# Performance work log

Hardware: AMD Instinct MI355X
Metric: run time of the kernel (lower is better)

The kernel has to match this reference:

```python
import jax, jax.numpy as jnp
import numpy as np

HIDDEN = 2048
NUM_HEAD = 32
GROUP = 8
HEAD_DIM = HIDDEN // NUM_HEAD  # 64
REP = NUM_HEAD // GROUP        # 4


def setup_inputs() -> dict:
    key = jax.random.key(0)
    ks = jax.random.split(key, 9)
    s = 0.02
    kv_dim = GROUP * HEAD_DIM
    return {
        "hidden_states": jax.random.normal(ks[0], (2, 2048, HIDDEN), dtype=jnp.float32),
        "Wq": jax.random.normal(ks[1], (HIDDEN, HIDDEN), dtype=jnp.float32) * s,
        "bq": jnp.zeros((HIDDEN,), dtype=jnp.float32),
        "Wk": jax.random.normal(ks[2], (HIDDEN, kv_dim), dtype=jnp.float32) * s,
        "bk": jnp.zeros((kv_dim,), dtype=jnp.float32),
        "Wv": jax.random.normal(ks[3], (HIDDEN, kv_dim), dtype=jnp.float32) * s,
        "bv": jnp.zeros((kv_dim,), dtype=jnp.float32),
        "Wo": jax.random.normal(ks[4], (HIDDEN, HIDDEN), dtype=jnp.float32) * s,
        "bo": jnp.zeros((HIDDEN,), dtype=jnp.float32),
    }


def reference(hidden_states, Wq, bq, Wk, bk, Wv, bv, Wo, bo):
    B, S, H = hidden_states.shape
    q = hidden_states @ Wq + bq                      # [B,S,H]
    k = hidden_states @ Wk + bk                      # [B,S,G*hd]
    v = hidden_states @ Wv + bv
    q = q.reshape(B, S, NUM_HEAD, HEAD_DIM).transpose(0, 2, 1, 3)   # [B,nh,S,hd]
    k = k.reshape(B, S, GROUP, HEAD_DIM).transpose(0, 2, 1, 3)      # [B,G,S,hd]
    v = v.reshape(B, S, GROUP, HEAD_DIM).transpose(0, 2, 1, 3)
    # expand KV heads: each group head repeated REP times contiguously
    k = jnp.repeat(k, REP, axis=1)                   # [B,nh,S,hd]
    v = jnp.repeat(v, REP, axis=1)
    scale = 1.0 / jnp.sqrt(jnp.float32(HEAD_DIM))
    scores = jnp.einsum("bhqd,bhkd->bhqk", q, k) * scale  # [B,nh,S,S]
    attn = jax.nn.softmax(scores, axis=-1)
    out = jnp.einsum("bhqk,bhkd->bhqd", attn, v)     # [B,nh,S,hd]
    out = out.transpose(0, 2, 1, 3).reshape(B, S, NUM_HEAD * HEAD_DIM)
    return out @ Wo + bo
```

## Files before the change

kernel.cpp:

```cpp
#include <hip/hip_runtime.h>
#include <hip/hip_bf16.h>

typedef __attribute__((ext_vector_type(8))) short bf16x8;
typedef __attribute__((ext_vector_type(4))) short bf16x4;
typedef __attribute__((ext_vector_type(4))) float f32x4;

__device__ __forceinline__ unsigned short f2bf(float f) {
  union { float f; unsigned int u; } v; v.f = f;
  unsigned int r = (v.u + 0x7fffu + ((v.u >> 16) & 1u)) >> 16;
  return (unsigned short)r;
}

__device__ __forceinline__ unsigned int pk2bf(float a, float b) {
  float2 t; t.x = a; t.y = b;
  __hip_bfloat162 h = __float22bfloat162_rn(t);
  union { __hip_bfloat162 h; unsigned int u; } cv; cv.h = h;
  return cv.u;
}

__device__ __forceinline__ void g2l16(unsigned short* lds, const unsigned short* g) {
  __builtin_amdgcn_global_load_lds(
      (const __attribute__((address_space(1))) unsigned int*)g,
      (__attribute__((address_space(3))) unsigned int*)lds, 16, 0, 0);
}


__global__ __launch_bounds__(256) void cast_hs_kernel(const float* __restrict__ in,
                                                      unsigned short* __restrict__ out) {
  size_t i = (size_t)blockIdx.x * 256 + threadIdx.x;
  float4 v = ((const float4*)in)[i];
  ushort4 o;
  o.x = f2bf(v.x); o.y = f2bf(v.y); o.z = f2bf(v.z); o.w = f2bf(v.w);
  ((ushort4*)out)[i] = o;
}

__global__ __launch_bounds__(256) void transpose_cast_kernel(const float* __restrict__ src,
                                                             unsigned short* __restrict__ dst,
                                                             int N) {
  __shared__ float tile[32][33];
  int n0 = blockIdx.x * 32, k0 = blockIdx.y * 32;
  int t = threadIdx.x;
  for (int i = 0; i < 4; ++i) {
    int linear = i * 256 + t;
    int kr = linear >> 5, nc = linear & 31;
    tile[kr][nc] = src[(size_t)(k0 + kr) * N + (n0 + nc)];
  }
  __syncthreads();
  for (int i = 0; i < 4; ++i) {
    int linear = i * 256 + t;
    int nr = linear >> 5, kc = linear & 31;
    dst[(size_t)(n0 + nr) * 2048 + (k0 + kc)] = f2bf(tile[kc][nr]);
  }
}


#define QSCALE 0.18033688011112042f

__global__ __launch_bounds__(256) void gemm_qkv_kernel(
    const unsigned short* __restrict__ A, const unsigned short* __restrict__ Bt,
    const float* __restrict__ bq, const float* __restrict__ bk, const float* __restrict__ bv,
    unsigned short* __restrict__ Qb, unsigned short* __restrict__ Kb,
    unsigned short* __restrict__ Vtb) {
  __shared__ __align__(16) unsigned short smem[128 * 136];
  unsigned short* sA = smem;
  unsigned short* sB = smem + 4096;
  const int K = 2048;
  int bm0 = blockIdx.y * 128, bn0 = blockIdx.x * 128;
  int t = threadIdx.x;
  int w = t >> 6, lane = t & 63, l16 = lane & 15, quad = lane >> 4;
  int wm = (w & 1) * 64, wn = (w >> 1) * 64;
  f32x4 zero = {0.f, 0.f, 0.f, 0.f};
  f32x4 acc[4][4];
  for (int mt = 0; mt < 4; ++mt)
    for (int nt = 0; nt < 4; ++nt) acc[mt][nt] = zero;

  for (int k0 = 0; k0 < K; k0 += 32) {
    for (int i = 0; i < 2; ++i) {
      int linear = i * 256 + t;
      int row = linear >> 2, kofs = (linear & 3) * 8;
      g2l16(sA + linear * 8, A + (size_t)(bm0 + row) * K + k0 + kofs);
      g2l16(sB + linear * 8, Bt + (size_t)(bn0 + row) * K + k0 + kofs);
    }
    __syncthreads();
    bf16x8 af[4], bfr[4];
    for (int mt = 0; mt < 4; ++mt)
      af[mt] = *(const bf16x8*)(sA + (wm + mt * 16 + l16) * 32 + quad * 8);
    for (int nt = 0; nt < 4; ++nt)
      bfr[nt] = *(const bf16x8*)(sB + (wn + nt * 16 + l16) * 32 + quad * 8);
    for (int mt = 0; mt < 4; ++mt)
      for (int nt = 0; nt < 4; ++nt)
        acc[mt][nt] = __builtin_amdgcn_mfma_f32_16x16x32_bf16(af[mt], bfr[nt], acc[mt][nt], 0, 0, 0);
    __syncthreads();
  }

  const int SP = 136;
  bool isV = (bn0 >= 2560);
  bool isQ = (bn0 < 2048);
  const float* bias = isQ ? bq : (bn0 < 2560 ? bk : bv);
  int nbase = isQ ? 0 : (bn0 < 2560 ? 2048 : 2560);

  for (int nt = 0; nt < 4; ++nt) {
    int nl = wn + nt * 16 + l16;
    float bb = bias[bn0 + nl - nbase];
    for (int mt = 0; mt < 4; ++mt)
      for (int r = 0; r < 4; ++r) {
        int ml = wm + mt * 16 + quad * 4 + r;
        float fv = acc[mt][nt][r] + bb;
        if (isQ) fv *= QSCALE;
        unsigned short val = f2bf(fv);
        if (isV) smem[nl * SP + ml] = val;
        else     smem[ml * SP + nl] = val;
      }
  }
  __syncthreads();

  int b = bm0 >> 11, s0 = bm0 & 2047;
  if (bn0 < 2048) {
    for (int i = 0; i < 8; ++i) {
      int idx = i * 256 + t;
      int sub = idx >> 10, s_l = (idx >> 3) & 127, dch = (idx & 7) * 8;
      bf16x8 v = *(const bf16x8*)(smem + s_l * SP + sub * 64 + dch);
      int n = bn0 + sub * 64 + dch;
      int h = n >> 6, d = n & 63;
      *(bf16x8*)(Qb + (((size_t)b * 32 + h) * 2048 + s0 + s_l) * 64 + d) = v;
    }
  } else if (bn0 < 2560) {
    for (int i = 0; i < 8; ++i) {
      int idx = i * 256 + t;
      int sub = idx >> 10, s_l = (idx >> 3) & 127, dch = (idx & 7) * 8;
      bf16x8 v = *(const bf16x8*)(smem + s_l * SP + sub * 64 + dch);
      int nn = bn0 + sub * 64 + dch - 2048;
      int g = nn >> 6, d = nn & 63;
      *(bf16x8*)(Kb + (((size_t)b * 8 + g) * 2048 + s0 + s_l) * 64 + d) = v;
    }
  } else {
    for (int i = 0; i < 8; ++i) {
      int idx = i * 256 + t;
      int nl = idx >> 4, sj = (idx & 15) * 8;
      bf16x8 v = *(const bf16x8*)(smem + nl * SP + sj);
      int nn = bn0 + nl - 2560;
      int g = nn >> 6, d = nn & 63;
      *(bf16x8*)(Vtb + (((size_t)b * 8 + g) * 64 + d) * 2048 + s0 + sj) = v;
    }
  }
}


__global__ __launch_bounds__(256) void attn_kernel(
    const unsigned short* __restrict__ Qb, const unsigned short* __restrict__ Kb,
    const unsigned short* __restrict__ Vtb, unsigned short* __restrict__ AttnB) {
  __shared__ __align__(16) unsigned short Kt[64 * 64];
  __shared__ __align__(16) unsigned short Vt[64 * 64];
  int qt = blockIdx.x, h = blockIdx.y, b = blockIdx.z;
  int g = h >> 2;
  int t = threadIdx.x, w = t >> 6, lane = t & 63, l16 = lane & 15, quad = lane >> 4;

  const unsigned short* qbase =
      Qb + (((size_t)b * 32 + h) * 2048 + qt * 64 + w * 16 + l16) * 64 + quad * 8;
  bf16x8 aQ0 = *(const bf16x8*)(qbase);
  bf16x8 aQ1 = *(const bf16x8*)(qbase + 32);

  const unsigned short* kbase = Kb + ((size_t)b * 8 + g) * (2048 * 64);
  const unsigned short* vbase = Vtb + ((size_t)b * 8 + g) * (64 * 2048);

  float l_acc = 0.f;
  f32x4 zero = {0.f, 0.f, 0.f, 0.f};
  f32x4 o[4];
  for (int dt = 0; dt < 4; ++dt) o[dt] = zero;

  for (int kb = 0; kb < 32; ++kb) {
    for (int i = 0; i < 2; ++i) {
      int linear = i * 256 + t;
      int row = linear & 63, c = linear >> 6;
      g2l16(Kt + linear * 8, kbase + (size_t)(kb * 64 + row) * 64 + c * 8);
      g2l16(Vt + linear * 8, vbase + (size_t)row * 2048 + kb * 64 + c * 8);
    }
    __syncthreads();

    for (int nt = 0; nt < 4; ++nt) {
      bf16x8 bk0 = *(const bf16x8*)(Kt + (quad * 64 + nt * 16 + l16) * 8);
      bf16x8 bk1 = *(const bf16x8*)(Kt + ((quad + 4) * 64 + nt * 16 + l16) * 8);
      f32x4 st = __builtin_amdgcn_mfma_f32_16x16x32_bf16(bk0, aQ0, zero, 0, 0, 0);
      st = __builtin_amdgcn_mfma_f32_16x16x32_bf16(bk1, aQ1, st, 0, 0, 0);

      float p0 = __builtin_amdgcn_exp2f(st[0] - 10.0f);
      float p1 = __builtin_amdgcn_exp2f(st[1] - 10.0f);
      float p2 = __builtin_amdgcn_exp2f(st[2] - 10.0f);
      float p3 = __builtin_amdgcn_exp2f(st[3] - 10.0f);
      l_acc += (p0 + p1) + (p2 + p3);

      union { unsigned int u[2]; bf16x4 v; } pa;
      pa.u[0] = pk2bf(p0, p1);
      pa.u[1] = pk2bf(p2, p3);

      int c = nt * 2 + (quad >> 1);
      int ho = (quad & 1) * 4;
      for (int dt = 0; dt < 4; ++dt) {
        bf16x4 bv = *(const bf16x4*)(Vt + (c * 64 + dt * 16 + l16) * 8 + ho);
        o[dt] = __builtin_amdgcn_mfma_f32_16x16x16bf16_1k(pa.v, bv, o[dt], 0, 0, 0);
      }
    }
    __syncthreads();
  }

  l_acc += __shfl_xor(l_acc, 16);
  l_acc += __shfl_xor(l_acc, 32);

  for (int r = 0; r < 4; ++r) {
    float lr = __shfl(l_acc, quad * 4 + r);
    float inv = 1.f / lr;
    int srow = qt * 64 + w * 16 + quad * 4 + r;
    size_t base = ((size_t)b * 2048 + srow) * 2048 + h * 64;
    for (int dt = 0; dt < 4; ++dt)
      AttnB[base + dt * 16 + l16] = f2bf(o[dt][r] * inv);
  }
}


__global__ __launch_bounds__(256) void gemm_out_kernel(
    const unsigned short* __restrict__ A, const unsigned short* __restrict__ Bt,
    const float* __restrict__ bo, float* __restrict__ out) {
  __shared__ __align__(16) unsigned short sA[128 * 32];
  __shared__ __align__(16) unsigned short sB[128 * 32];
  const int K = 2048;
  int bm0 = blockIdx.y * 128, bn0 = blockIdx.x * 128;
  int t = threadIdx.x;
  int w = t >> 6, lane = t & 63, l16 = lane & 15, quad = lane >> 4;
  int wm = (w & 1) * 64, wn = (w >> 1) * 64;
  f32x4 zero = {0.f, 0.f, 0.f, 0.f};
  f32x4 acc[4][4];
  for (int mt = 0; mt < 4; ++mt)
    for (int nt = 0; nt < 4; ++nt) acc[mt][nt] = zero;

  for (int k0 = 0; k0 < K; k0 += 32) {
    for (int i = 0; i < 2; ++i) {
      int linear = i * 256 + t;
      int row = linear >> 2, kofs = (linear & 3) * 8;
      g2l16(sA + linear * 8, A + (size_t)(bm0 + row) * K + k0 + kofs);
      g2l16(sB + linear * 8, Bt + (size_t)(bn0 + row) * K + k0 + kofs);
    }
    __syncthreads();
    bf16x8 af[4], bfr[4];
    for (int mt = 0; mt < 4; ++mt)
      af[mt] = *(const bf16x8*)(sA + (wm + mt * 16 + l16) * 32 + quad * 8);
    for (int nt = 0; nt < 4; ++nt)
      bfr[nt] = *(const bf16x8*)(sB + (wn + nt * 16 + l16) * 32 + quad * 8);
    for (int mt = 0; mt < 4; ++mt)
      for (int nt = 0; nt < 4; ++nt)
        acc[mt][nt] = __builtin_amdgcn_mfma_f32_16x16x32_bf16(af[mt], bfr[nt], acc[mt][nt], 0, 0, 0);
    __syncthreads();
  }

  for (int nt = 0; nt < 4; ++nt) {
    int n = bn0 + wn + nt * 16 + l16;
    float bias = bo[n];
    for (int mt = 0; mt < 4; ++mt)
      for (int r = 0; r < 4; ++r) {
        int m = bm0 + wm + mt * 16 + quad * 4 + r;
        out[(size_t)m * 2048 + n] = acc[mt][nt][r] + bias;
      }
  }
}


extern "C" void kernel_launch(void* const* d_in, const int* in_sizes, int n_in,
                              void* d_out, int out_size, void* d_ws, size_t ws_size,
                              hipStream_t stream) {
  const float* hs = (const float*)d_in[0];
  const float* Wq = (const float*)d_in[1];
  const float* bq = (const float*)d_in[2];
  const float* Wk = (const float*)d_in[3];
  const float* bk = (const float*)d_in[4];
  const float* Wv = (const float*)d_in[5];
  const float* bv = (const float*)d_in[6];
  const float* Wo = (const float*)d_in[7];
  const float* bo = (const float*)d_in[8];
  float* out = (float*)d_out;

  char* ws = (char*)d_ws;
  unsigned short* hsb   = (unsigned short*)(ws);
  unsigned short* Wqkv  = (unsigned short*)(ws + 16777216);
  unsigned short* WoT   = (unsigned short*)(ws + 29360128);
  unsigned short* Qb    = (unsigned short*)(ws + 37748736);
  unsigned short* Kb    = (unsigned short*)(ws + 54525952);
  unsigned short* Vtb   = (unsigned short*)(ws + 58720256);
  unsigned short* AttnB = (unsigned short*)(ws + 62914560);

  hipLaunchKernelGGL(cast_hs_kernel, dim3(8192), dim3(256), 0, stream, hs, hsb);
  hipLaunchKernelGGL(transpose_cast_kernel, dim3(64, 64), dim3(256), 0, stream, Wq, Wqkv, 2048);
  hipLaunchKernelGGL(transpose_cast_kernel, dim3(16, 64), dim3(256), 0, stream,
                     Wk, Wqkv + (size_t)2048 * 2048, 512);
  hipLaunchKernelGGL(transpose_cast_kernel, dim3(16, 64), dim3(256), 0, stream,
                     Wv, Wqkv + (size_t)2560 * 2048, 512);
  hipLaunchKernelGGL(transpose_cast_kernel, dim3(64, 64), dim3(256), 0, stream, Wo, WoT, 2048);
  hipLaunchKernelGGL(gemm_qkv_kernel, dim3(24, 32), dim3(256), 0, stream,
                     hsb, Wqkv, bq, bk, bv, Qb, Kb, Vtb);
  hipLaunchKernelGGL(attn_kernel, dim3(32, 32, 2), dim3(256), 0, stream, Qb, Kb, Vtb, AttnB);
  hipLaunchKernelGGL(gemm_out_kernel, dim3(16, 32), dim3(256), 0, stream, AttnB, WoT, bo, out);
}
```

Before: 371.1 us.

## Double GEMM K-tile with XOR-swizzled LDS, widen attention KV block, merge transposes

```diff
diff --git a/kernel.cpp b/kernel.cpp
--- a/kernel.cpp
+++ b/kernel.cpp
@@ -34,10 +34,18 @@
   ((ushort4*)out)[i] = o;
 }
 
-__global__ __launch_bounds__(256) void transpose_cast_kernel(const float* __restrict__ src,
-                                                             unsigned short* __restrict__ dst,
-                                                             int N) {
+__global__ __launch_bounds__(256) void transpose_all_kernel(
+    const float* __restrict__ Wq, const float* __restrict__ Wk,
+    const float* __restrict__ Wv, const float* __restrict__ Wo,
+    unsigned short* __restrict__ Wqkv, unsigned short* __restrict__ WoT) {
   __shared__ float tile[32][33];
+  int z = blockIdx.z;
+  const float* src; unsigned short* dst; int N;
+  if (z == 0)      { src = Wq; dst = Wqkv;                          N = 2048; }
+  else if (z == 1) { src = Wk; dst = Wqkv + (size_t)2048 * 2048;    N = 512; }
+  else if (z == 2) { src = Wv; dst = Wqkv + (size_t)2560 * 2048;    N = 512; }
+  else             { src = Wo; dst = WoT;                           N = 2048; }
+  if (blockIdx.x * 32 >= N) return;
   int n0 = blockIdx.x * 32, k0 = blockIdx.y * 32;
   int t = threadIdx.x;
   for (int i = 0; i < 4; ++i) {
@@ -63,33 +71,37 @@
     unsigned short* __restrict__ Vtb) {
   __shared__ __align__(16) unsigned short smem[128 * 136];
   unsigned short* sA = smem;
-  unsigned short* sB = smem + 4096;
+  unsigned short* sB = smem + 8192;
   const int K = 2048;
   int bm0 = blockIdx.y * 128, bn0 = blockIdx.x * 128;
   int t = threadIdx.x;
   int w = t >> 6, lane = t & 63, l16 = lane & 15, quad = lane >> 4;
   int wm = (w & 1) * 64, wn = (w >> 1) * 64;
+  int x7 = l16 & 7;
   f32x4 zero = {0.f, 0.f, 0.f, 0.f};
   f32x4 acc[4][4];
   for (int mt = 0; mt < 4; ++mt)
     for (int nt = 0; nt < 4; ++nt) acc[mt][nt] = zero;
 
-  for (int k0 = 0; k0 < K; k0 += 32) {
-    for (int i = 0; i < 2; ++i) {
+  for (int k0 = 0; k0 < K; k0 += 64) {
+    for (int i = 0; i < 4; ++i) {
       int linear = i * 256 + t;
-      int row = linear >> 2, kofs = (linear & 3) * 8;
-      g2l16(sA + linear * 8, A + (size_t)(bm0 + row) * K + k0 + kofs);
-      g2l16(sB + linear * 8, Bt + (size_t)(bn0 + row) * K + k0 + kofs);
-    }
-    __syncthreads();
-    bf16x8 af[4], bfr[4];
-    for (int mt = 0; mt < 4; ++mt)
-      af[mt] = *(const bf16x8*)(sA + (wm + mt * 16 + l16) * 32 + quad * 8);
-    for (int nt = 0; nt < 4; ++nt)
-      bfr[nt] = *(const bf16x8*)(sB + (wn + nt * 16 + l16) * 32 + quad * 8);
-    for (int mt = 0; mt < 4; ++mt)
+      int row = linear >> 3, cg = ((linear & 7) ^ (row & 7)) * 8;
+      g2l16(sA + linear * 8, A + (size_t)(bm0 + row) * K + k0 + cg);
+      g2l16(sB + linear * 8, Bt + (size_t)(bn0 + row) * K + k0 + cg);
+    }
+    __syncthreads();
+    for (int s = 0; s < 2; ++s) {
+      bf16x8 af[4], bfr[4];
+      int ck = ((s * 4 + quad) ^ x7) * 8;
+      for (int mt = 0; mt < 4; ++mt)
+        af[mt] = *(const bf16x8*)(sA + (wm + mt * 16 + l16) * 64 + ck);
       for (int nt = 0; nt < 4; ++nt)
-        acc[mt][nt] = __builtin_amdgcn_mfma_f32_16x16x32_bf16(af[mt], bfr[nt], acc[mt][nt], 0, 0, 0);
+        bfr[nt] = *(const bf16x8*)(sB + (wn + nt * 16 + l16) * 64 + ck);
+      for (int mt = 0; mt < 4; ++mt)
+        for (int nt = 0; nt < 4; ++nt)
+          acc[mt][nt] = __builtin_amdgcn_mfma_f32_16x16x32_bf16(af[mt], bfr[nt], acc[mt][nt], 0, 0, 0);
+    }
     __syncthreads();
   }
 
@@ -149,8 +161,8 @@
 __global__ __launch_bounds__(256) void attn_kernel(
     const unsigned short* __restrict__ Qb, const unsigned short* __restrict__ Kb,
     const unsigned short* __restrict__ Vtb, unsigned short* __restrict__ AttnB) {
-  __shared__ __align__(16) unsigned short Kt[64 * 64];
-  __shared__ __align__(16) unsigned short Vt[64 * 64];
+  __shared__ __align__(16) unsigned short Kt[8 * 128 * 8];
+  __shared__ __align__(16) unsigned short Vt[16 * 64 * 8];
   int qt = blockIdx.x, h = blockIdx.y, b = blockIdx.z;
   int g = h >> 2;
   int t = threadIdx.x, w = t >> 6, lane = t & 63, l16 = lane & 15, quad = lane >> 4;
@@ -168,18 +180,19 @@
   f32x4 o[4];
   for (int dt = 0; dt < 4; ++dt) o[dt] = zero;
 
-  for (int kb = 0; kb < 32; ++kb) {
-    for (int i = 0; i < 2; ++i) {
+  for (int kb = 0; kb < 16; ++kb) {
+    for (int i = 0; i < 4; ++i) {
       int linear = i * 256 + t;
-      int row = linear & 63, c = linear >> 6;
-      g2l16(Kt + linear * 8, kbase + (size_t)(kb * 64 + row) * 64 + c * 8);
-      g2l16(Vt + linear * 8, vbase + (size_t)row * 2048 + kb * 64 + c * 8);
-    }
-    __syncthreads();
-
-    for (int nt = 0; nt < 4; ++nt) {
-      bf16x8 bk0 = *(const bf16x8*)(Kt + (quad * 64 + nt * 16 + l16) * 8);
-      bf16x8 bk1 = *(const bf16x8*)(Kt + ((quad + 4) * 64 + nt * 16 + l16) * 8);
+      int krow = linear & 127, kc = linear >> 7;
+      g2l16(Kt + linear * 8, kbase + (size_t)(kb * 128 + krow) * 64 + kc * 8);
+      int vd = linear & 63, vc = linear >> 6;
+      g2l16(Vt + linear * 8, vbase + (size_t)vd * 2048 + kb * 128 + vc * 8);
+    }
+    __syncthreads();
+
+    for (int nt = 0; nt < 8; ++nt) {
+      bf16x8 bk0 = *(const bf16x8*)(Kt + (quad * 128 + nt * 16 + l16) * 8);
+      bf16x8 bk1 = *(const bf16x8*)(Kt + ((quad + 4) * 128 + nt * 16 + l16) * 8);
       f32x4 st = __builtin_amdgcn_mfma_f32_16x16x32_bf16(bk0, aQ0, zero, 0, 0, 0);
       st = __builtin_amdgcn_mfma_f32_16x16x32_bf16(bk1, aQ1, st, 0, 0, 0);
 
@@ -220,34 +233,38 @@
 __global__ __launch_bounds__(256) void gemm_out_kernel(
     const unsigned short* __restrict__ A, const unsigned short* __restrict__ Bt,
     const float* __restrict__ bo, float* __restrict__ out) {
-  __shared__ __align__(16) unsigned short sA[128 * 32];
-  __shared__ __align__(16) unsigned short sB[128 * 32];
+  __shared__ __align__(16) unsigned short sA[128 * 64];
+  __shared__ __align__(16) unsigned short sB[128 * 64];
   const int K = 2048;
   int bm0 = blockIdx.y * 128, bn0 = blockIdx.x * 128;
   int t = threadIdx.x;
   int w = t >> 6, lane = t & 63, l16 = lane & 15, quad = lane >> 4;
   int wm = (w & 1) * 64, wn = (w >> 1) * 64;
+  int x7 = l16 & 7;
   f32x4 zero = {0.f, 0.f, 0.f, 0.f};
   f32x4 acc[4][4];
   for (int mt = 0; mt < 4; ++mt)
     for (int nt = 0; nt < 4; ++nt) acc[mt][nt] = zero;
 
-  for (int k0 = 0; k0 < K; k0 += 32) {
-    for (int i = 0; i < 2; ++i) {
+  for (int k0 = 0; k0 < K; k0 += 64) {
+    for (int i = 0; i < 4; ++i) {
       int linear = i * 256 + t;
-      int row = linear >> 2, kofs = (linear & 3) * 8;
-      g2l16(sA + linear * 8, A + (size_t)(bm0 + row) * K + k0 + kofs);
-      g2l16(sB + linear * 8, Bt + (size_t)(bn0 + row) * K + k0 + kofs);
-    }
-    __syncthreads();
-    bf16x8 af[4], bfr[4];
-    for (int mt = 0; mt < 4; ++mt)
-      af[mt] = *(const bf16x8*)(sA + (wm + mt * 16 + l16) * 32 + quad * 8);
-    for (int nt = 0; nt < 4; ++nt)
-      bfr[nt] = *(const bf16x8*)(sB + (wn + nt * 16 + l16) * 32 + quad * 8);
-    for (int mt = 0; mt < 4; ++mt)
+      int row = linear >> 3, cg = ((linear & 7) ^ (row & 7)) * 8;
+      g2l16(sA + linear * 8, A + (size_t)(bm0 + row) * K + k0 + cg);
+      g2l16(sB + linear * 8, Bt + (size_t)(bn0 + row) * K + k0 + cg);
+    }
+    __syncthreads();
+    for (int s = 0; s < 2; ++s) {
+      bf16x8 af[4], bfr[4];
+      int ck = ((s * 4 + quad) ^ x7) * 8;
+      for (int mt = 0; mt < 4; ++mt)
+        af[mt] = *(const bf16x8*)(sA + (wm + mt * 16 + l16) * 64 + ck);
       for (int nt = 0; nt < 4; ++nt)
-        acc[mt][nt] = __builtin_amdgcn_mfma_f32_16x16x32_bf16(af[mt], bfr[nt], acc[mt][nt], 0, 0, 0);
+        bfr[nt] = *(const bf16x8*)(sB + (wn + nt * 16 + l16) * 64 + ck);
+      for (int mt = 0; mt < 4; ++mt)
+        for (int nt = 0; nt < 4; ++nt)
+          acc[mt][nt] = __builtin_amdgcn_mfma_f32_16x16x32_bf16(af[mt], bfr[nt], acc[mt][nt], 0, 0, 0);
+    }
     __syncthreads();
   }
 
@@ -287,12 +304,8 @@
   unsigned short* AttnB = (unsigned short*)(ws + 62914560);
 
   hipLaunchKernelGGL(cast_hs_kernel, dim3(8192), dim3(256), 0, stream, hs, hsb);
-  hipLaunchKernelGGL(transpose_cast_kernel, dim3(64, 64), dim3(256), 0, stream, Wq, Wqkv, 2048);
-  hipLaunchKernelGGL(transpose_cast_kernel, dim3(16, 64), dim3(256), 0, stream,
-                     Wk, Wqkv + (size_t)2048 * 2048, 512);
-  hipLaunchKernelGGL(transpose_cast_kernel, dim3(16, 64), dim3(256), 0, stream,
-                     Wv, Wqkv + (size_t)2560 * 2048, 512);
-  hipLaunchKernelGGL(transpose_cast_kernel, dim3(64, 64), dim3(256), 0, stream, Wo, WoT, 2048);
+  hipLaunchKernelGGL(transpose_all_kernel, dim3(64, 64, 4), dim3(256), 0, stream,
+                     Wq, Wk, Wv, Wo, Wqkv, WoT);
   hipLaunchKernelGGL(gemm_qkv_kernel, dim3(24, 32), dim3(256), 0, stream,
                      hsb, Wqkv, bq, bk, bv, Qb, Kb, Vtb);
   hipLaunchKernelGGL(attn_kernel, dim3(32, 32, 2), dim3(256), 0, stream, Qb, Kb, Vtb, AttnB);
```

New measurement: 395.9 us. 6.7% more time.
